# Kernel optimization log

Measured on AMD Instinct MI355X. Metric: run time of the kernel, lower is better.

Reference implementation:

```python
import jax, jax.numpy as jnp
import numpy as np

N_NODES = 50000
N_EDGES = 800000
NUM_GRAPHS = 512
IN_DIM = 128
HID = 128
OUT_DIM = 1


def setup_inputs() -> dict:
    key = jax.random.key(0)
    ks = jax.random.split(key, 8)
    x = jax.random.normal(ks[0], (N_NODES, IN_DIM), dtype=jnp.float32)
    edge_index = jax.random.randint(ks[1], (2, N_EDGES), 0, N_NODES, dtype=jnp.int64)
    batch = jnp.sort(jax.random.randint(ks[2], (N_NODES,), 0, NUM_GRAPHS, dtype=jnp.int64))
    s1 = 1.0 / np.sqrt(IN_DIM)
    s2 = 1.0 / np.sqrt(HID)
    W1 = jax.random.normal(ks[3], (IN_DIM, HID), dtype=jnp.float32) * s1
    b1 = jnp.zeros((HID,), dtype=jnp.float32)
    W2 = jax.random.normal(ks[4], (HID, HID), dtype=jnp.float32) * s2
    b2 = jnp.zeros((HID,), dtype=jnp.float32)
    Wl = jax.random.normal(ks[5], (HID, OUT_DIM), dtype=jnp.float32) * s2
    bl = jnp.zeros((OUT_DIM,), dtype=jnp.float32)
    return {"x": x, "edge_index": edge_index, "batch": batch,
            "W1": W1, "b1": b1, "W2": W2, "b2": b2, "Wl": Wl, "bl": bl}


def _gcn_conv(x, src, dst, norm, W, b):
    # GCNConv: D^{-1/2}(A+I)D^{-1/2} X W + b (self-loops already in src/dst)
    h = x @ W                                    # [N, H]
    msg = h[src] * norm[:, None]                 # gather + edge-normalize
    agg = jax.ops.segment_sum(msg, dst, num_segments=N_NODES)  # scatter-add
    return agg + b


def reference(x, edge_index, batch, W1, b1, W2, b2, Wl, bl):
    loops = jnp.arange(N_NODES, dtype=edge_index.dtype)
    src = jnp.concatenate([edge_index[0], loops])
    dst = jnp.concatenate([edge_index[1], loops])
    deg = jax.ops.segment_sum(jnp.ones_like(dst, dtype=x.dtype), dst, num_segments=N_NODES)
    dinv = jax.lax.rsqrt(deg)                    # deg >= 1 due to self-loops
    norm = dinv[src] * dinv[dst]                 # symmetric normalization per edge

    h = jax.nn.relu(_gcn_conv(x, src, dst, norm, W1, b1))
    h = jax.nn.relu(_gcn_conv(h, src, dst, norm, W2, b2))

    # global_mean_pool over graph ids
    sums = jax.ops.segment_sum(h, batch, num_segments=NUM_GRAPHS)
    cnts = jax.ops.segment_sum(jnp.ones((N_NODES,), dtype=h.dtype), batch, num_segments=NUM_GRAPHS)
    pooled = sums / jnp.maximum(cnts, 1.0)[:, None]

    out = jax.nn.sigmoid(pooled @ Wl + bl)       # [G, 1]
    return out.squeeze(1)                        # [G]
```

## Files before the change

kernel.cpp:

```cpp
#include <hip/hip_runtime.h>
#include <hip/hip_bf16.h>

#define N_NODES 50000
#define N_EDGES 800000
#define NUM_GRAPHS 512
#define MAXDEG 64
#define EPB 4096
#define P1_BLOCKS 196
#define NBUCK 256
#define NPB 196

typedef short short8 __attribute__((ext_vector_type(8)));
typedef unsigned short u16x8 __attribute__((ext_vector_type(8)));
typedef float f32x4 __attribute__((ext_vector_type(4)));

__device__ __forceinline__ unsigned short f2bu(float f) {
    __hip_bfloat16 h = __float2bfloat16(f);
    return *reinterpret_cast<unsigned short*>(&h);
}
__device__ __forceinline__ float bu2f(unsigned short u) {
    unsigned int v = ((unsigned int)u) << 16;
    float f;
    __builtin_memcpy(&f, &v, 4);
    return f;
}

__global__ __launch_bounds__(256) void bin_k(const int* __restrict__ ei,
                                             unsigned int* __restrict__ staging,
                                             int* __restrict__ cnts_tbl,
                                             int* __restrict__ offs_tbl,
                                             unsigned short* __restrict__ hs) {
    __shared__ unsigned int st[EPB];
    __shared__ int cnt[NBUCK], cur[NBUCK], scan[NBUCK];
    int b = blockIdx.x, t = threadIdx.x;
    if (b == 0 && t < 64)
        ((unsigned int*)(hs + (size_t)N_NODES * 128))[t] = 0u;
    cnt[t] = 0;
    __syncthreads();

    int e0 = b * EPB;
    int srcv[16], dstv[16], bk[16];
#pragma unroll
    for (int k = 0; k < 16; ++k) {
        int e = e0 + k * 256 + t;
        bool ok = e < N_EDGES;
        srcv[k] = ok ? ei[e] : 0;
        dstv[k] = ok ? ei[N_EDGES + e] : 0;
        bk[k] = ok ? (dstv[k] / NPB) : -1;
        if (ok) atomicAdd(&cnt[bk[k]], 1);
    }
    __syncthreads();
    scan[t] = cnt[t];
    __syncthreads();
    for (int off = 1; off < 256; off <<= 1) {
        int u = t >= off ? scan[t - off] : 0;
        __syncthreads();
        scan[t] += u;
        __syncthreads();
    }
    int excl = scan[t] - cnt[t];
    cur[t] = excl;
    cnts_tbl[t * P1_BLOCKS + b] = cnt[t];
    offs_tbl[t * P1_BLOCKS + b] = excl;
    __syncthreads();
#pragma unroll
    for (int k = 0; k < 16; ++k) {
        if (bk[k] >= 0) {
            int pos = atomicAdd(&cur[bk[k]], 1);
            int dl = dstv[k] - bk[k] * NPB;
            st[pos] = (unsigned int)srcv[k] | ((unsigned int)dl << 16);
        }
    }
    __syncthreads();
    unsigned int* gout = staging + (size_t)b * EPB;
    for (int i = t; i < EPB; i += 256) gout[i] = st[i];
}

__global__ __launch_bounds__(256) void adjbuild_k(const unsigned int* __restrict__ staging,
                                                  const int* __restrict__ cnts_tbl,
                                                  const int* __restrict__ offs_tbl,
                                                  unsigned short* __restrict__ adj,
                                                  int* __restrict__ cnt,
                                                  float* __restrict__ dinv,
                                                  const float* __restrict__ W1,
                                                  const float* __restrict__ W2,
                                                  unsigned short* __restrict__ W1t,
                                                  unsigned short* __restrict__ W2t) {
    int b = blockIdx.x, t = threadIdx.x;
    if (b >= NBUCK) {
        int wb = b - NBUCK;
        const float* W = wb < 64 ? W1 : W2;
        unsigned short* Wt = wb < 64 ? W1t : W2t;
        int idx = (wb & 63) * 256 + t;
        int k = idx >> 7, n = idx & 127;
        Wt[n * 128 + k] = f2bu(W[idx]);
        return;
    }
    __shared__ unsigned short adjL[NPB * MAXDEG];
    __shared__ int cntL[NPB];
    __shared__ int segStart[P1_BLOCKS + 1];
    __shared__ int segOff[P1_BLOCKS];
    __shared__ int tmp[256];

    if (t < NPB) cntL[t] = 0;
    int c = t < P1_BLOCKS ? cnts_tbl[b * P1_BLOCKS + t] : 0;
    if (t < P1_BLOCKS) segOff[t] = offs_tbl[b * P1_BLOCKS + t];
    tmp[t] = c;
    __syncthreads();
    for (int off = 1; off < 256; off <<= 1) {
        int u = t >= off ? tmp[t - off] : 0;
        __syncthreads();
        tmp[t] += u;
        __syncthreads();
    }
    if (t < P1_BLOCKS) segStart[t] = tmp[t] - c;
    if (t == 0) segStart[P1_BLOCKS] = tmp[P1_BLOCKS - 1];
    __syncthreads();

    int T = segStart[P1_BLOCKS];
    for (int f = t; f < T; f += 256) {
        int lo = 0, hi = P1_BLOCKS;
        while (hi - lo > 1) {
            int m = (lo + hi) >> 1;
            if (segStart[m] <= f) lo = m; else hi = m;
        }
        unsigned int p = staging[(size_t)lo * EPB + segOff[lo] + (f - segStart[lo])];
        int src = p & 0xFFFF;
        int dl = p >> 16;
        int slot = atomicAdd(&cntL[dl], 1);
        if (slot < MAXDEG - 1) adjL[dl * MAXDEG + slot] = (unsigned short)src;
    }
    __syncthreads();

    int nodeBase = b * NPB;
    if (t < NPB) {
        int node = nodeBase + t;
        int cc = cntL[t];
        int ec = cc < MAXDEG - 1 ? cc : MAXDEG - 1;
        adjL[t * MAXDEG + ec] = (unsigned short)node;
        int tot = ec + 1, tot4 = (tot + 3) & ~3;
        for (int s = tot; s < tot4; ++s) adjL[t * MAXDEG + s] = (unsigned short)N_NODES;
        if (node < N_NODES) {
            cnt[node] = cc;
            dinv[node] = rsqrtf((float)cc + 1.0f);
        }
    }
    __syncthreads();
    unsigned int* g = (unsigned int*)(adj + (size_t)nodeBase * MAXDEG);
    const unsigned int* l = (const unsigned int*)adjL;
    for (int i = t; i < NPB * MAXDEG / 2; i += 256) g[i] = l[i];
}

template <bool F32A>
__global__ __launch_bounds__(256) void gemm_k(const void* __restrict__ Ap,
                                              const unsigned short* __restrict__ Wt,
                                              const float* __restrict__ dinv,
                                              unsigned short* __restrict__ C) {
    __shared__ unsigned short Wl[128 * 136];
    int t = threadIdx.x;
    for (int idx = t; idx < 2048; idx += 256) {
        int n = idx >> 4, c = idx & 15;
        *(u16x8*)(Wl + n * 136 + c * 8) = *(const u16x8*)(Wt + n * 128 + c * 8);
    }
    __syncthreads();

    int wave = t >> 6, lane = t & 63, quad = lane >> 4, ln = lane & 15;
    int rb = blockIdx.x * 128 + wave * 16;

    short8 a[2][4];
#pragma unroll
    for (int mt = 0; mt < 2; ++mt) {
        int r = rb + mt * 64 + ln;
        r = r < N_NODES ? r : N_NODES - 1;
        if (F32A) {
            const float* arow = (const float*)Ap + (size_t)r * 128 + quad * 8;
#pragma unroll
            for (int ks = 0; ks < 4; ++ks) {
                float4 v0 = *(const float4*)(arow + ks * 32);
                float4 v1 = *(const float4*)(arow + ks * 32 + 4);
                short8 av;
                av[0] = (short)f2bu(v0.x); av[1] = (short)f2bu(v0.y);
                av[2] = (short)f2bu(v0.z); av[3] = (short)f2bu(v0.w);
                av[4] = (short)f2bu(v1.x); av[5] = (short)f2bu(v1.y);
                av[6] = (short)f2bu(v1.z); av[7] = (short)f2bu(v1.w);
                a[mt][ks] = av;
            }
        } else {
            const unsigned short* arow = (const unsigned short*)Ap + (size_t)r * 128 + quad * 8;
#pragma unroll
            for (int ks = 0; ks < 4; ++ks) a[mt][ks] = *(const short8*)(arow + ks * 32);
        }
    }

    f32x4 acc[2][8];
#pragma unroll
    for (int mt = 0; mt < 2; ++mt)
#pragma unroll
        for (int ct = 0; ct < 8; ++ct) acc[mt][ct] = (f32x4){0.f, 0.f, 0.f, 0.f};

#pragma unroll
    for (int ks = 0; ks < 4; ++ks)
#pragma unroll
        for (int ct = 0; ct < 8; ++ct) {
            short8 b = *(const short8*)(Wl + (ct * 16 + ln) * 136 + ks * 32 + quad * 8);
            acc[0][ct] = __builtin_amdgcn_mfma_f32_16x16x32_bf16(a[0][ks], b, acc[0][ct], 0, 0, 0);
            acc[1][ct] = __builtin_amdgcn_mfma_f32_16x16x32_bf16(a[1][ks], b, acc[1][ct], 0, 0, 0);
        }

#pragma unroll
    for (int mt = 0; mt < 2; ++mt) {
#pragma unroll
        for (int rr = 0; rr < 4; ++rr) {
            int r = rb + mt * 64 + quad * 4 + rr;
            if (r >= N_NODES) continue;
            float dv = dinv[r];
#pragma unroll
            for (int ct = 0; ct < 8; ++ct)
                C[(size_t)r * 128 + ct * 16 + ln] = f2bu(acc[mt][ct][rr] * dv);
        }
    }
}

__global__ __launch_bounds__(256) void agg_k(const unsigned short* __restrict__ hs,
                                             const unsigned short* __restrict__ adj,
                                             const int* __restrict__ cnt,
                                             const float* __restrict__ dinv,
                                             const float* __restrict__ bias,
                                             unsigned short* __restrict__ out) {
    int wave = threadIdx.x >> 6, lane = threadIdx.x & 63;
    int node = blockIdx.x * 4 + wave;
    int quad = lane >> 4, fl = lane & 15;
    int idx = (int)adj[node * MAXDEG + lane];
    int c = cnt[node];
    int ec = c < MAXDEG - 1 ? c : MAXDEG - 1;
    int iters = (ec + 1 + 3) >> 2;

    float acc[8];
#pragma unroll
    for (int j = 0; j < 8; ++j) acc[j] = 0.f;

    for (int i = 0; i < iters; ++i) {
        int s = __shfl(idx, i * 4 + quad, 64);
        u16x8 v = *(const u16x8*)(hs + (size_t)s * 128 + fl * 8);
#pragma unroll
        for (int j = 0; j < 8; ++j) acc[j] += bu2f(v[j]);
    }

#pragma unroll
    for (int j = 0; j < 8; ++j) {
        acc[j] += __shfl_xor(acc[j], 16, 64);
        acc[j] += __shfl_xor(acc[j], 32, 64);
    }

    if (quad == 0) {
        float dv = dinv[node];
        float4 b0 = *(const float4*)(bias + fl * 8);
        float4 b1 = *(const float4*)(bias + fl * 8 + 4);
        u16x8 o;
        o[0] = f2bu(fmaxf(acc[0] * dv + b0.x, 0.f));
        o[1] = f2bu(fmaxf(acc[1] * dv + b0.y, 0.f));
        o[2] = f2bu(fmaxf(acc[2] * dv + b0.z, 0.f));
        o[3] = f2bu(fmaxf(acc[3] * dv + b0.w, 0.f));
        o[4] = f2bu(fmaxf(acc[4] * dv + b1.x, 0.f));
        o[5] = f2bu(fmaxf(acc[5] * dv + b1.y, 0.f));
        o[6] = f2bu(fmaxf(acc[6] * dv + b1.z, 0.f));
        o[7] = f2bu(fmaxf(acc[7] * dv + b1.w, 0.f));
        *(u16x8*)(out + (size_t)node * 128 + fl * 8) = o;
    }
}

__device__ __forceinline__ int lb(const int* a, int n, int v) {
    int lo = 0, hi = n;
    while (lo < hi) {
        int m = (lo + hi) >> 1;
        if (a[m] < v) lo = m + 1;
        else hi = m;
    }
    return lo;
}

__global__ __launch_bounds__(256) void pool_k(const unsigned short* __restrict__ h2,
                                              const int* __restrict__ batch,
                                              const float* __restrict__ Wl,
                                              const float* __restrict__ bl,
                                              float* __restrict__ out) {
    __shared__ float buf[256];
    __shared__ float part[2];
    int g = blockIdx.x, t = threadIdx.x;
    int f = t & 127, stripe = t >> 7;
    int lo = lb(batch, N_NODES, g), hi = lb(batch, N_NODES, g + 1);
    float s = 0.f;
    for (int r = lo + stripe; r < hi; r += 2)
        s += bu2f(h2[(size_t)r * 128 + f]);
    buf[t] = s;
    __syncthreads();
    if (t < 128) {
        float cf = (float)(hi - lo);
        float pooled = (buf[t] + buf[t + 128]) / fmaxf(cf, 1.f);
        float p = pooled * Wl[t];
#pragma unroll
        for (int o = 32; o > 0; o >>= 1) p += __shfl_down(p, o, 64);
        if ((t & 63) == 0) part[t >> 6] = p;
    }
    __syncthreads();
    if (t == 0) out[g] = 1.f / (1.f + expf(-(part[0] + part[1] + bl[0])));
}

extern "C" void kernel_launch(void* const* d_in, const int* in_sizes, int n_in,
                              void* d_out, int out_size, void* d_ws, size_t ws_size,
                              hipStream_t stream) {
    const float* x = (const float*)d_in[0];
    const int* ei = (const int*)d_in[1];
    const int* batch = (const int*)d_in[2];
    const float* W1 = (const float*)d_in[3];
    const float* b1 = (const float*)d_in[4];
    const float* W2 = (const float*)d_in[5];
    const float* b2 = (const float*)d_in[6];
    const float* Wl = (const float*)d_in[7];
    const float* bl = (const float*)d_in[8];
    float* out = (float*)d_out;

    char* ws = (char*)d_ws;
    unsigned int* staging = (unsigned int*)(ws + 0x0);
    int* cnts_tbl = (int*)(ws + 0x310000);
    int* offs_tbl = (int*)(ws + 0x341000);
    unsigned short* adj = (unsigned short*)(ws + 0x372000);
    int* cnt = (int*)(ws + 0x992000);
    float* dinv = (float*)(ws + 0x9C3000);
    unsigned short* W1t = (unsigned short*)(ws + 0x9F4000);
    unsigned short* W2t = (unsigned short*)(ws + 0x9FC000);
    unsigned short* hs = (unsigned short*)(ws + 0xA04000);
    unsigned short* h1b = (unsigned short*)(ws + 0x1640000);
    unsigned short* h2b = (unsigned short*)(ws + 0x2280000);

    bin_k<<<P1_BLOCKS, 256, 0, stream>>>(ei, staging, cnts_tbl, offs_tbl, hs);
    adjbuild_k<<<NBUCK + 128, 256, 0, stream>>>(staging, cnts_tbl, offs_tbl,
                                                adj, cnt, dinv, W1, W2, W1t, W2t);

    gemm_k<true><<<(N_NODES + 127) / 128, 256, 0, stream>>>(x, W1t, dinv, hs);
    agg_k<<<N_NODES / 4, 256, 0, stream>>>(hs, adj, cnt, dinv, b1, h1b);

    gemm_k<false><<<(N_NODES + 127) / 128, 256, 0, stream>>>(h1b, W2t, dinv, hs);
    agg_k<<<N_NODES / 4, 256, 0, stream>>>(hs, adj, cnt, dinv, b2, h2b);

    pool_k<<<NUM_GRAPHS, 256, 0, stream>>>(h2b, batch, Wl, bl, out);
}
```

Baseline: 221.3 us.

## Fuse layer-1 aggregation with layer-2 GEMM and unroll gather loops

Layer-1 neighbor aggregation now feeds the layer-2 bf16 MFMA GEMM inside one kernel. Each block of 16 nodes stages its aggregated rows in LDS and multiplies them against W2 held in shared memory, so the h1 intermediate never makes a round trip through global memory and one launch disappears. The gather loops are unrolled by two so each wave has more loads in flight, and the pooling kernel is reworked to read packed pairs and reduce across four waves. The cost is that every block of only 16 rows reloads the full 32 KB W2 into LDS, and the larger LDS footprint may lower occupancy for the gather-bound part.

Result: faster. 206.1 us (-6.9%).

```diff
diff --git a/kernel.cpp b/kernel.cpp
--- a/kernel.cpp
+++ b/kernel.cpp
@@ -29,12 +29,15 @@
                                              unsigned int* __restrict__ staging,
                                              int* __restrict__ cnts_tbl,
                                              int* __restrict__ offs_tbl,
-                                             unsigned short* __restrict__ hs) {
+                                             unsigned short* __restrict__ hs1,
+                                             unsigned short* __restrict__ hs2) {
     __shared__ unsigned int st[EPB];
     __shared__ int cnt[NBUCK], cur[NBUCK], scan[NBUCK];
     int b = blockIdx.x, t = threadIdx.x;
     if (b == 0 && t < 64)
-        ((unsigned int*)(hs + (size_t)N_NODES * 128))[t] = 0u;
+        ((unsigned int*)(hs1 + (size_t)N_NODES * 128))[t] = 0u;
+    if (b == 1 && t < 64)
+        ((unsigned int*)(hs2 + (size_t)N_NODES * 128))[t] = 0u;
     cnt[t] = 0;
     __syncthreads();
 
@@ -151,8 +154,7 @@
     for (int i = t; i < NPB * MAXDEG / 2; i += 256) g[i] = l[i];
 }
 
-template <bool F32A>
-__global__ __launch_bounds__(256) void gemm_k(const void* __restrict__ Ap,
+__global__ __launch_bounds__(256) void gemm_k(const float* __restrict__ Ap,
                                               const unsigned short* __restrict__ Wt,
                                               const float* __restrict__ dinv,
                                               unsigned short* __restrict__ C) {
@@ -172,23 +174,17 @@
     for (int mt = 0; mt < 2; ++mt) {
         int r = rb + mt * 64 + ln;
         r = r < N_NODES ? r : N_NODES - 1;
-        if (F32A) {
-            const float* arow = (const float*)Ap + (size_t)r * 128 + quad * 8;
-#pragma unroll
-            for (int ks = 0; ks < 4; ++ks) {
-                float4 v0 = *(const float4*)(arow + ks * 32);
-                float4 v1 = *(const float4*)(arow + ks * 32 + 4);
-                short8 av;
-                av[0] = (short)f2bu(v0.x); av[1] = (short)f2bu(v0.y);
-                av[2] = (short)f2bu(v0.z); av[3] = (short)f2bu(v0.w);
-                av[4] = (short)f2bu(v1.x); av[5] = (short)f2bu(v1.y);
-                av[6] = (short)f2bu(v1.z); av[7] = (short)f2bu(v1.w);
-                a[mt][ks] = av;
-            }
-        } else {
-            const unsigned short* arow = (const unsigned short*)Ap + (size_t)r * 128 + quad * 8;
-#pragma unroll
-            for (int ks = 0; ks < 4; ++ks) a[mt][ks] = *(const short8*)(arow + ks * 32);
+        const float* arow = Ap + (size_t)r * 128 + quad * 8;
+#pragma unroll
+        for (int ks = 0; ks < 4; ++ks) {
+            float4 v0 = *(const float4*)(arow + ks * 32);
+            float4 v1 = *(const float4*)(arow + ks * 32 + 4);
+            short8 av;
+            av[0] = (short)f2bu(v0.x); av[1] = (short)f2bu(v0.y);
+            av[2] = (short)f2bu(v0.z); av[3] = (short)f2bu(v0.w);
+            av[4] = (short)f2bu(v1.x); av[5] = (short)f2bu(v1.y);
+            av[6] = (short)f2bu(v1.z); av[7] = (short)f2bu(v1.w);
+            a[mt][ks] = av;
         }
     }
 
@@ -219,6 +215,104 @@
                 C[(size_t)r * 128 + ct * 16 + ln] = f2bu(acc[mt][ct][rr] * dv);
         }
     }
+}
+
+__global__ __launch_bounds__(256) void agg_gemm_k(const unsigned short* __restrict__ hs1,
+                                                  const unsigned short* __restrict__ adj,
+                                                  const int* __restrict__ cnt,
+                                                  const float* __restrict__ dinv,
+                                                  const float* __restrict__ bias,
+                                                  const unsigned short* __restrict__ W2t,
+                                                  unsigned short* __restrict__ hs2) {
+    __shared__ unsigned short Wl[128 * 136];
+    __shared__ unsigned short h1t[16 * 136];
+    int t = threadIdx.x, wave = t >> 6, lane = t & 63;
+    int quad = lane >> 4, fl = lane & 15;
+    for (int idx = t; idx < 2048; idx += 256) {
+        int n = idx >> 4, c = idx & 15;
+        *(u16x8*)(Wl + n * 136 + c * 8) = *(const u16x8*)(W2t + n * 128 + c * 8);
+    }
+    int nb = blockIdx.x * 16;
+
+    float4 b0 = *(const float4*)(bias + fl * 8);
+    float4 b1f = *(const float4*)(bias + fl * 8 + 4);
+
+#pragma unroll
+    for (int q = 0; q < 4; ++q) {
+        int lr = wave * 4 + q;
+        int node = nb + lr;
+        int idxv = (int)adj[node * MAXDEG + lane];
+        int c = cnt[node];
+        int ec = c < MAXDEG - 1 ? c : MAXDEG - 1;
+        int iters = (ec + 4) >> 2;
+
+        float acc[8];
+#pragma unroll
+        for (int j = 0; j < 8; ++j) acc[j] = 0.f;
+
+        int i = 0;
+        for (; i + 2 <= iters; i += 2) {
+            int s0 = __shfl(idxv, i * 4 + quad, 64);
+            int s1 = __shfl(idxv, i * 4 + 4 + quad, 64);
+            u16x8 v0 = *(const u16x8*)(hs1 + (size_t)s0 * 128 + fl * 8);
+            u16x8 v1 = *(const u16x8*)(hs1 + (size_t)s1 * 128 + fl * 8);
+#pragma unroll
+            for (int j = 0; j < 8; ++j) acc[j] += bu2f(v0[j]) + bu2f(v1[j]);
+        }
+        if (i < iters) {
+            int s0 = __shfl(idxv, i * 4 + quad, 64);
+            u16x8 v0 = *(const u16x8*)(hs1 + (size_t)s0 * 128 + fl * 8);
+#pragma unroll
+            for (int j = 0; j < 8; ++j) acc[j] += bu2f(v0[j]);
+        }
+#pragma unroll
+        for (int j = 0; j < 8; ++j) {
+            acc[j] += __shfl_xor(acc[j], 16, 64);
+            acc[j] += __shfl_xor(acc[j], 32, 64);
+        }
+        if (quad == 0) {
+            float dv = dinv[node];
+            u16x8 o;
+            o[0] = f2bu(fmaxf(acc[0] * dv + b0.x, 0.f));
+            o[1] = f2bu(fmaxf(acc[1] * dv + b0.y, 0.f));
+            o[2] = f2bu(fmaxf(acc[2] * dv + b0.z, 0.f));
+            o[3] = f2bu(fmaxf(acc[3] * dv + b0.w, 0.f));
+            o[4] = f2bu(fmaxf(acc[4] * dv + b1f.x, 0.f));
+            o[5] = f2bu(fmaxf(acc[5] * dv + b1f.y, 0.f));
+            o[6] = f2bu(fmaxf(acc[6] * dv + b1f.z, 0.f));
+            o[7] = f2bu(fmaxf(acc[7] * dv + b1f.w, 0.f));
+            *(u16x8*)(h1t + lr * 136 + fl * 8) = o;
+        }
+    }
+    __syncthreads();
+
+    int ln = fl;
+    short8 a[4];
+#pragma unroll
+    for (int ks = 0; ks < 4; ++ks)
+        a[ks] = *(const short8*)(h1t + ln * 136 + ks * 32 + quad * 8);
+
+    f32x4 acc2[2];
+    acc2[0] = (f32x4){0.f, 0.f, 0.f, 0.f};
+    acc2[1] = (f32x4){0.f, 0.f, 0.f, 0.f};
+#pragma unroll
+    for (int ks = 0; ks < 4; ++ks)
+#pragma unroll
+        for (int ct = 0; ct < 2; ++ct) {
+            short8 b = *(const short8*)(Wl + (wave * 32 + ct * 16 + ln) * 136 + ks * 32 + quad * 8);
+            acc2[ct] = __builtin_amdgcn_mfma_f32_16x16x32_bf16(a[ks], b, acc2[ct], 0, 0, 0);
+        }
+
+    float dvr[4];
+#pragma unroll
+    for (int rr = 0; rr < 4; ++rr) dvr[rr] = dinv[nb + quad * 4 + rr];
+#pragma unroll
+    for (int ct = 0; ct < 2; ++ct)
+#pragma unroll
+        for (int rr = 0; rr < 4; ++rr) {
+            int node = nb + quad * 4 + rr;
+            hs2[(size_t)node * 128 + wave * 32 + ct * 16 + ln] = f2bu(acc2[ct][rr] * dvr[rr]);
+        }
 }
 
 __global__ __launch_bounds__(256) void agg_k(const unsigned short* __restrict__ hs,
@@ -233,17 +327,26 @@
     int idx = (int)adj[node * MAXDEG + lane];
     int c = cnt[node];
     int ec = c < MAXDEG - 1 ? c : MAXDEG - 1;
-    int iters = (ec + 1 + 3) >> 2;
+    int iters = (ec + 4) >> 2;
 
     float acc[8];
 #pragma unroll
     for (int j = 0; j < 8; ++j) acc[j] = 0.f;
 
-    for (int i = 0; i < iters; ++i) {
-        int s = __shfl(idx, i * 4 + quad, 64);
-        u16x8 v = *(const u16x8*)(hs + (size_t)s * 128 + fl * 8);
-#pragma unroll
-        for (int j = 0; j < 8; ++j) acc[j] += bu2f(v[j]);
+    int i = 0;
+    for (; i + 2 <= iters; i += 2) {
+        int s0 = __shfl(idx, i * 4 + quad, 64);
+        int s1 = __shfl(idx, i * 4 + 4 + quad, 64);
+        u16x8 v0 = *(const u16x8*)(hs + (size_t)s0 * 128 + fl * 8);
+        u16x8 v1 = *(const u16x8*)(hs + (size_t)s1 * 128 + fl * 8);
+#pragma unroll
+        for (int j = 0; j < 8; ++j) acc[j] += bu2f(v0[j]) + bu2f(v1[j]);
+    }
+    if (i < iters) {
+        int s0 = __shfl(idx, i * 4 + quad, 64);
+        u16x8 v0 = *(const u16x8*)(hs + (size_t)s0 * 128 + fl * 8);
+#pragma unroll
+        for (int j = 0; j < 8; ++j) acc[j] += bu2f(v0[j]);
     }
 
 #pragma unroll
@@ -285,25 +388,27 @@
                                               const float* __restrict__ bl,
                                               float* __restrict__ out) {
     __shared__ float buf[256];
-    __shared__ float part[2];
+    __shared__ float part[4];
     int g = blockIdx.x, t = threadIdx.x;
-    int f = t & 127, stripe = t >> 7;
+    int fp = t & 63, stripe = t >> 6;
     int lo = lb(batch, N_NODES, g), hi = lb(batch, N_NODES, g + 1);
-    float s = 0.f;
-    for (int r = lo + stripe; r < hi; r += 2)
-        s += bu2f(h2[(size_t)r * 128 + f]);
-    buf[t] = s;
-    __syncthreads();
-    if (t < 128) {
+    float s0 = 0.f, s1 = 0.f;
+    for (int r = lo + stripe; r < hi; r += 4) {
+        unsigned int u = *(const unsigned int*)(h2 + (size_t)r * 128 + fp * 2);
+        s0 += bu2f((unsigned short)(u & 0xFFFF));
+        s1 += bu2f((unsigned short)(u >> 16));
+    }
+    float p = s0 * Wl[fp * 2] + s1 * Wl[fp * 2 + 1];
+#pragma unroll
+    for (int o = 32; o > 0; o >>= 1) p += __shfl_down(p, o, 64);
+    if ((t & 63) == 0) part[t >> 6] = p;
+    __syncthreads();
+    if (t == 0) {
         float cf = (float)(hi - lo);
-        float pooled = (buf[t] + buf[t + 128]) / fmaxf(cf, 1.f);
-        float p = pooled * Wl[t];
-#pragma unroll
-        for (int o = 32; o > 0; o >>= 1) p += __shfl_down(p, o, 64);
-        if ((t & 63) == 0) part[t >> 6] = p;
-    }
-    __syncthreads();
-    if (t == 0) out[g] = 1.f / (1.f + expf(-(part[0] + part[1] + bl[0])));
+        float z = (part[0] + part[1] + part[2] + part[3]) / fmaxf(cf, 1.f) + bl[0];
+        out[g] = 1.f / (1.f + expf(-z));
+    }
+    (void)buf;
 }
 
 extern "C" void kernel_launch(void* const* d_in, const int* in_sizes, int n_in,
@@ -329,19 +434,17 @@
     float* dinv = (float*)(ws + 0x9C3000);
     unsigned short* W1t = (unsigned short*)(ws + 0x9F4000);
     unsigned short* W2t = (unsigned short*)(ws + 0x9FC000);
-    unsigned short* hs = (unsigned short*)(ws + 0xA04000);
-    unsigned short* h1b = (unsigned short*)(ws + 0x1640000);
+    unsigned short* hs1 = (unsigned short*)(ws + 0xA04000);
+    unsigned short* hs2 = (unsigned short*)(ws + 0x1640000);
     unsigned short* h2b = (unsigned short*)(ws + 0x2280000);
 
-    bin_k<<<P1_BLOCKS, 256, 0, stream>>>(ei, staging, cnts_tbl, offs_tbl, hs);
+    bin_k<<<P1_BLOCKS, 256, 0, stream>>>(ei, staging, cnts_tbl, offs_tbl, hs1, hs2);
     adjbuild_k<<<NBUCK + 128, 256, 0, stream>>>(staging, cnts_tbl, offs_tbl,
                                                 adj, cnt, dinv, W1, W2, W1t, W2t);
 
-    gemm_k<true><<<(N_NODES + 127) / 128, 256, 0, stream>>>(x, W1t, dinv, hs);
-    agg_k<<<N_NODES / 4, 256, 0, stream>>>(hs, adj, cnt, dinv, b1, h1b);
-
-    gemm_k<false><<<(N_NODES + 127) / 128, 256, 0, stream>>>(h1b, W2t, dinv, hs);
-    agg_k<<<N_NODES / 4, 256, 0, stream>>>(hs, adj, cnt, dinv, b2, h2b);
+    gemm_k<<<(N_NODES + 127) / 128, 256, 0, stream>>>(x, W1t, dinv, hs1);
+    agg_gemm_k<<<N_NODES / 16, 256, 0, stream>>>(hs1, adj, cnt, dinv, b1, W2t, hs2);
+    agg_k<<<N_NODES / 4, 256, 0, stream>>>(hs2, adj, cnt, dinv, b2, h2b);
 
     pool_k<<<NUM_GRAPHS, 256, 0, stream>>>(h2b, batch, Wl, bl, out);
 }
```

## Split aggregation into feature chunks and fuse layer-2 aggregation with output dot

Applied to the files above, without the earlier changes.

Aggregation kernels now use a 2D grid over four 32-feature chunks. Each wave processes 16 neighbours per iteration, with 4 lanes per neighbour row. The first two neighbour loads are issued up front, and padding uses a prefilled sentinel index pointing at a zeroed row. The second aggregation computes the per-node dot product with Wl directly, writing one partial per chunk instead of the full h2 tensor. The final pooling kernel then only sums scalars per graph. This removes the h2 write and re-read and aims to raise memory parallelism in the gather, at the cost of four times as many blocks each re-reading adjacency.

Result: slower. 296.3 us (+33.9%).

```diff
diff --git a/kernel.cpp b/kernel.cpp
--- a/kernel.cpp
+++ b/kernel.cpp
@@ -29,12 +29,15 @@
                                              unsigned int* __restrict__ staging,
                                              int* __restrict__ cnts_tbl,
                                              int* __restrict__ offs_tbl,
-                                             unsigned short* __restrict__ hs) {
+                                             unsigned short* __restrict__ hs1,
+                                             unsigned short* __restrict__ hs2) {
     __shared__ unsigned int st[EPB];
     __shared__ int cnt[NBUCK], cur[NBUCK], scan[NBUCK];
     int b = blockIdx.x, t = threadIdx.x;
     if (b == 0 && t < 64)
-        ((unsigned int*)(hs + (size_t)N_NODES * 128))[t] = 0u;
+        ((unsigned int*)(hs1 + (size_t)N_NODES * 128))[t] = 0u;
+    if (b == 1 && t < 64)
+        ((unsigned int*)(hs2 + (size_t)N_NODES * 128))[t] = 0u;
     cnt[t] = 0;
     __syncthreads();
 
@@ -103,6 +106,8 @@
     __shared__ int tmp[256];
 
     if (t < NPB) cntL[t] = 0;
+    for (int i = t; i < NPB * MAXDEG / 2; i += 256)
+        ((unsigned int*)adjL)[i] = 0xC350C350u;
     int c = t < P1_BLOCKS ? cnts_tbl[b * P1_BLOCKS + t] : 0;
     if (t < P1_BLOCKS) segOff[t] = offs_tbl[b * P1_BLOCKS + t];
     tmp[t] = c;
@@ -138,8 +143,6 @@
         int cc = cntL[t];
         int ec = cc < MAXDEG - 1 ? cc : MAXDEG - 1;
         adjL[t * MAXDEG + ec] = (unsigned short)node;
-        int tot = ec + 1, tot4 = (tot + 3) & ~3;
-        for (int s = tot; s < tot4; ++s) adjL[t * MAXDEG + s] = (unsigned short)N_NODES;
         if (node < N_NODES) {
             cnt[node] = cc;
             dinv[node] = rsqrtf((float)cc + 1.0f);
@@ -221,41 +224,48 @@
     }
 }
 
-__global__ __launch_bounds__(256) void agg_k(const unsigned short* __restrict__ hs,
-                                             const unsigned short* __restrict__ adj,
-                                             const int* __restrict__ cnt,
-                                             const float* __restrict__ dinv,
-                                             const float* __restrict__ bias,
-                                             unsigned short* __restrict__ out) {
-    int wave = threadIdx.x >> 6, lane = threadIdx.x & 63;
+__global__ __launch_bounds__(256) void agg1_k(const unsigned short* __restrict__ hs1,
+                                              const unsigned short* __restrict__ adj,
+                                              const int* __restrict__ cnt,
+                                              const float* __restrict__ dinv,
+                                              const float* __restrict__ bias,
+                                              unsigned short* __restrict__ h1) {
+    int t = threadIdx.x, wave = t >> 6, lane = t & 63;
+    int g = lane >> 2, sub = lane & 3;
     int node = blockIdx.x * 4 + wave;
-    int quad = lane >> 4, fl = lane & 15;
-    int idx = (int)adj[node * MAXDEG + lane];
+    int chunk = blockIdx.y;
+    int av = (int)adj[node * MAXDEG + lane];
     int c = cnt[node];
     int ec = c < MAXDEG - 1 ? c : MAXDEG - 1;
-    int iters = (ec + 1 + 3) >> 2;
-
+    int tot = ec + 1;
+    int iters = (tot + 15) >> 4;
+    const unsigned short* base = hs1 + chunk * 32 + sub * 8;
+
+    int s0 = __shfl(av, g, 64);
+    int s1 = __shfl(av, 16 + g, 64);
+    u16x8 v0 = *(const u16x8*)(base + (size_t)s0 * 128);
+    u16x8 v1 = *(const u16x8*)(base + (size_t)s1 * 128);
     float acc[8];
 #pragma unroll
-    for (int j = 0; j < 8; ++j) acc[j] = 0.f;
-
-    for (int i = 0; i < iters; ++i) {
-        int s = __shfl(idx, i * 4 + quad, 64);
-        u16x8 v = *(const u16x8*)(hs + (size_t)s * 128 + fl * 8);
+    for (int j = 0; j < 8; ++j) acc[j] = bu2f(v0[j]) + bu2f(v1[j]);
+    for (int i = 2; i < iters; ++i) {
+        int s = __shfl(av, i * 16 + g, 64);
+        u16x8 v = *(const u16x8*)(base + (size_t)s * 128);
 #pragma unroll
         for (int j = 0; j < 8; ++j) acc[j] += bu2f(v[j]);
     }
-
 #pragma unroll
     for (int j = 0; j < 8; ++j) {
+        acc[j] += __shfl_xor(acc[j], 4, 64);
+        acc[j] += __shfl_xor(acc[j], 8, 64);
         acc[j] += __shfl_xor(acc[j], 16, 64);
         acc[j] += __shfl_xor(acc[j], 32, 64);
     }
-
-    if (quad == 0) {
+    if (lane < 4) {
         float dv = dinv[node];
-        float4 b0 = *(const float4*)(bias + fl * 8);
-        float4 b1 = *(const float4*)(bias + fl * 8 + 4);
+        const float* bp = bias + chunk * 32 + lane * 8;
+        float4 b0 = *(const float4*)bp;
+        float4 b1 = *(const float4*)(bp + 4);
         u16x8 o;
         o[0] = f2bu(fmaxf(acc[0] * dv + b0.x, 0.f));
         o[1] = f2bu(fmaxf(acc[1] * dv + b0.y, 0.f));
@@ -265,8 +275,66 @@
         o[5] = f2bu(fmaxf(acc[5] * dv + b1.y, 0.f));
         o[6] = f2bu(fmaxf(acc[6] * dv + b1.z, 0.f));
         o[7] = f2bu(fmaxf(acc[7] * dv + b1.w, 0.f));
-        *(u16x8*)(out + (size_t)node * 128 + fl * 8) = o;
-    }
+        *(u16x8*)(h1 + (size_t)node * 128 + chunk * 32 + lane * 8) = o;
+    }
+}
+
+__global__ __launch_bounds__(256) void agg2dot_k(const unsigned short* __restrict__ hs2,
+                                                 const unsigned short* __restrict__ adj,
+                                                 const int* __restrict__ cnt,
+                                                 const float* __restrict__ dinv,
+                                                 const float* __restrict__ bias,
+                                                 const float* __restrict__ Wl,
+                                                 float* __restrict__ pnode) {
+    int t = threadIdx.x, wave = t >> 6, lane = t & 63;
+    int g = lane >> 2, sub = lane & 3;
+    int node = blockIdx.x * 4 + wave;
+    int chunk = blockIdx.y;
+    int av = (int)adj[node * MAXDEG + lane];
+    int c = cnt[node];
+    int ec = c < MAXDEG - 1 ? c : MAXDEG - 1;
+    int tot = ec + 1;
+    int iters = (tot + 15) >> 4;
+    const unsigned short* base = hs2 + chunk * 32 + sub * 8;
+
+    int s0 = __shfl(av, g, 64);
+    int s1 = __shfl(av, 16 + g, 64);
+    u16x8 v0 = *(const u16x8*)(base + (size_t)s0 * 128);
+    u16x8 v1 = *(const u16x8*)(base + (size_t)s1 * 128);
+    float acc[8];
+#pragma unroll
+    for (int j = 0; j < 8; ++j) acc[j] = bu2f(v0[j]) + bu2f(v1[j]);
+    for (int i = 2; i < iters; ++i) {
+        int s = __shfl(av, i * 16 + g, 64);
+        u16x8 v = *(const u16x8*)(base + (size_t)s * 128);
+#pragma unroll
+        for (int j = 0; j < 8; ++j) acc[j] += bu2f(v[j]);
+    }
+#pragma unroll
+    for (int j = 0; j < 8; ++j) {
+        acc[j] += __shfl_xor(acc[j], 4, 64);
+        acc[j] += __shfl_xor(acc[j], 8, 64);
+        acc[j] += __shfl_xor(acc[j], 16, 64);
+        acc[j] += __shfl_xor(acc[j], 32, 64);
+    }
+    float dv = dinv[node];
+    const float* bp = bias + chunk * 32 + sub * 8;
+    const float* wp = Wl + chunk * 32 + sub * 8;
+    float4 b0 = *(const float4*)bp;
+    float4 b1 = *(const float4*)(bp + 4);
+    float4 w0 = *(const float4*)wp;
+    float4 w1 = *(const float4*)(wp + 4);
+    float p = fmaxf(acc[0] * dv + b0.x, 0.f) * w0.x
+            + fmaxf(acc[1] * dv + b0.y, 0.f) * w0.y
+            + fmaxf(acc[2] * dv + b0.z, 0.f) * w0.z
+            + fmaxf(acc[3] * dv + b0.w, 0.f) * w0.w
+            + fmaxf(acc[4] * dv + b1.x, 0.f) * w1.x
+            + fmaxf(acc[5] * dv + b1.y, 0.f) * w1.y
+            + fmaxf(acc[6] * dv + b1.z, 0.f) * w1.z
+            + fmaxf(acc[7] * dv + b1.w, 0.f) * w1.w;
+    p += __shfl_xor(p, 1, 64);
+    p += __shfl_xor(p, 2, 64);
+    if (lane == 0) pnode[chunk * N_NODES + node] = p;
 }
 
 __device__ __forceinline__ int lb(const int* a, int n, int v) {
@@ -279,31 +347,23 @@
     return lo;
 }
 
-__global__ __launch_bounds__(256) void pool_k(const unsigned short* __restrict__ h2,
+__global__ __launch_bounds__(64) void final_k(const float* __restrict__ pnode,
                                               const int* __restrict__ batch,
-                                              const float* __restrict__ Wl,
                                               const float* __restrict__ bl,
                                               float* __restrict__ out) {
-    __shared__ float buf[256];
-    __shared__ float part[2];
     int g = blockIdx.x, t = threadIdx.x;
-    int f = t & 127, stripe = t >> 7;
     int lo = lb(batch, N_NODES, g), hi = lb(batch, N_NODES, g + 1);
     float s = 0.f;
-    for (int r = lo + stripe; r < hi; r += 2)
-        s += bu2f(h2[(size_t)r * 128 + f]);
-    buf[t] = s;
-    __syncthreads();
-    if (t < 128) {
+    for (int r = lo + t; r < hi; r += 64)
+        s += (pnode[r] + pnode[N_NODES + r])
+           + (pnode[2 * N_NODES + r] + pnode[3 * N_NODES + r]);
+#pragma unroll
+    for (int o = 32; o > 0; o >>= 1) s += __shfl_down(s, o, 64);
+    if (t == 0) {
         float cf = (float)(hi - lo);
-        float pooled = (buf[t] + buf[t + 128]) / fmaxf(cf, 1.f);
-        float p = pooled * Wl[t];
-#pragma unroll
-        for (int o = 32; o > 0; o >>= 1) p += __shfl_down(p, o, 64);
-        if ((t & 63) == 0) part[t >> 6] = p;
-    }
-    __syncthreads();
-    if (t == 0) out[g] = 1.f / (1.f + expf(-(part[0] + part[1] + bl[0])));
+        float z = s / fmaxf(cf, 1.f) + bl[0];
+        out[g] = 1.f / (1.f + expf(-z));
+    }
 }
 
 extern "C" void kernel_launch(void* const* d_in, const int* in_sizes, int n_in,
@@ -329,19 +389,19 @@
     float* dinv = (float*)(ws + 0x9C3000);
     unsigned short* W1t = (unsigned short*)(ws + 0x9F4000);
     unsigned short* W2t = (unsigned short*)(ws + 0x9FC000);
-    unsigned short* hs = (unsigned short*)(ws + 0xA04000);
-    unsigned short* h1b = (unsigned short*)(ws + 0x1640000);
-    unsigned short* h2b = (unsigned short*)(ws + 0x2280000);
-
-    bin_k<<<P1_BLOCKS, 256, 0, stream>>>(ei, staging, cnts_tbl, offs_tbl, hs);
+    float* pnode = (float*)(ws + 0xA04000);
+    unsigned short* hs1 = (unsigned short*)(ws + 0xAC8000);
+    unsigned short* h1 = (unsigned short*)(ws + 0x1710000);
+    unsigned short* hs2 = (unsigned short*)(ws + 0x2350000);
+
+    bin_k<<<P1_BLOCKS, 256, 0, stream>>>(ei, staging, cnts_tbl, offs_tbl, hs1, hs2);
     adjbuild_k<<<NBUCK + 128, 256, 0, stream>>>(staging, cnts_tbl, offs_tbl,
                                                 adj, cnt, dinv, W1, W2, W1t, W2t);
 
-    gemm_k<true><<<(N_NODES + 127) / 128, 256, 0, stream>>>(x, W1t, dinv, hs);
-    agg_k<<<N_NODES / 4, 256, 0, stream>>>(hs, adj, cnt, dinv, b1, h1b);
-
-    gemm_k<false><<<(N_NODES + 127) / 128, 256, 0, stream>>>(h1b, W2t, dinv, hs);
-    agg_k<<<N_NODES / 4, 256, 0, stream>>>(hs, adj, cnt, dinv, b2, h2b);
-
-    pool_k<<<NUM_GRAPHS, 256, 0, stream>>>(h2b, batch, Wl, bl, out);
-}
+    gemm_k<true><<<(N_NODES + 127) / 128, 256, 0, stream>>>(x, W1t, dinv, hs1);
+    agg1_k<<<dim3(N_NODES / 4, 4), 256, 0, stream>>>(hs1, adj, cnt, dinv, b1, h1);
+    gemm_k<false><<<(N_NODES + 127) / 128, 256, 0, stream>>>(h1, W2t, dinv, hs2);
+    agg2dot_k<<<dim3(N_NODES / 4, 4), 256, 0, stream>>>(hs2, adj, cnt, dinv, b2, Wl, pnode);
+
+    final_k<<<NUM_GRAPHS, 64, 0, stream>>>(pnode, batch, bl, out);
+}
```
